# Kernel optimization log

Hardware: AMD Instinct MI355X
Metric: run time of the kernel (lower is better)

## Reference

```python
import jax, jax.numpy as jnp
import numpy as np

B, C, H, W = 512, 64, 32, 64
NUM_NODE = 128


def setup_inputs() -> dict:
    key = jax.random.key(0)
    ks = jax.random.split(key, 11)
    f = jnp.float32
    def nrm(k, shape, s):
        return jax.random.normal(k, shape, f) * s
    return {
        "x":   jax.random.normal(ks[0], (B, C, H, W), f),
        "w11": nrm(ks[1], (32, 64, 1, 1), 0.1), "b11": nrm(ks[2], (32,), 0.05),
        "w12": nrm(ks[3], (16, 32, 3, 3), 0.1), "b12": nrm(ks[4], (16,), 0.05),
        "w21": nrm(ks[5], (8, 16, 1, 1), 0.1),  "b21": nrm(ks[6], (8,), 0.05),
        "w22": nrm(ks[7], (4, 8, 3, 3), 0.1),   "b22": nrm(ks[8], (4,), 0.05),
        "fcw": nrm(ks[9], (2 * NUM_NODE, 32 * 64 * 4), 0.05),
        "fcb": nrm(ks[10], (2 * NUM_NODE,), 0.05),
    }


def _conv_relu(x, w, b, pad):
    y = jax.lax.conv_general_dilated(
        x, w, window_strides=(1, 1), padding=[(pad, pad), (pad, pad)],
        dimension_numbers=("NCHW", "OIHW", "NCHW"))
    return jax.nn.relu(y + b[None, :, None, None])


def reference(x, w11, b11, w12, b12, w21, b21, w22, b22, fcw, fcb):
    # --- GraphGen3: conv stack -> fc -> n_Sigmoid -> [B, N, 2] ---
    h = _conv_relu(x, w11, b11, 0)
    h = _conv_relu(h, w12, b12, 1)
    h = _conv_relu(h, w21, b21, 0)
    h = _conv_relu(h, w22, b22, 1)          # [B, 4, 32, 64]
    z = h.reshape(h.shape[0], -1) @ fcw.T + fcb  # [B, 2N]
    c01 = jax.nn.sigmoid(3.0 * z).reshape(x.shape[0], -1, 2)  # n_Sigmoid(x, 3)
    # --- get_coord: scale normalized coords to pixel range ---
    Hd, Wd = x.shape[2], x.shape[3]
    coord = c01 * jnp.array([Hd - 1, Wd - 1], x.dtype)  # [B, N, 2]
    # --- th_batch_map_coordinates: clamp, corner gather, bilinear lerp ---
    ch = jnp.clip(coord[..., 0], 0.0, Hd - 1)
    cw = jnp.clip(coord[..., 1], 0.0, Wd - 1)
    h0 = jnp.floor(ch).astype(jnp.int32); h1 = jnp.ceil(ch).astype(jnp.int32)
    w0 = jnp.floor(cw).astype(jnp.int32); w1 = jnp.ceil(cw).astype(jnp.int32)
    bidx = jnp.arange(x.shape[0])[:, None]  # [B, 1]
    def gv(hi, wi):
        return x[bidx, :, hi, wi]           # gather -> [B, N, C]
    v_lt = gv(h0, w0); v_rt = gv(h1, w0)
    v_lb = gv(h0, w1); v_rb = gv(h1, w1)
    oh = (ch - h0.astype(x.dtype))[..., None]
    ow = (cw - w0.astype(x.dtype))[..., None]
    vt = v_lt + oh * (v_rt - v_lt)
    vb = v_lb + oh * (v_rb - v_lb)
    graph_feat = vt + ow * (vb - vt)        # [B, N, C] (matches permute(0,2,1))
    return graph_feat, coord
```

## Files before the change

kernel.cpp:

```cpp
#include <hip/hip_runtime.h>
#include <cstdint>

#define BATCH 512
#define CIN   64
#define HH    32
#define WW    64
#define HW    2048
#define C1    32
#define C2    16
#define C3    8
#define C4    4
#define NOUT  256
#define KFC   8192
#define NODES 128
#define KS    32
#define GF_SIZE (BATCH * NODES * CIN)

typedef __attribute__((ext_vector_type(8))) short bfrag;
typedef __attribute__((ext_vector_type(4))) float ffrag;

__device__ __forceinline__ ushort bf_trunc(float f) { return (ushort)(__float_as_uint(f) >> 16); }
__device__ __forceinline__ float  bf_truncf(float f) { return __uint_as_float(__float_as_uint(f) & 0xffff0000u); }
__device__ __forceinline__ ushort f2bf(float f) {
  uint32_t u = __float_as_uint(f);
  return (ushort)((u + 0x7fffu + ((u >> 16) & 1u)) >> 16);
}
__device__ __forceinline__ uint32_t pack2(float a, float b) {
  return (uint32_t)f2bf(a) | ((uint32_t)f2bf(b) << 16);
}
__device__ __forceinline__ uint32_t packhi2(float a, float b) {
  return (uint32_t)bf_trunc(a) | ((uint32_t)bf_trunc(b) << 16);
}

__global__ __launch_bounds__(256) void k_conv12(
    const float* __restrict__ x, const float* __restrict__ w11, const float* __restrict__ b11,
    const float* __restrict__ w12, const float* __restrict__ b12,
    float* __restrict__ h2, int b0)
{
  __shared__ __align__(16) char h1s[10 * 66 * 64];
  const int tid = threadIdx.x;
  const int l   = tid & 63;
  const int wv  = tid >> 6;
  const int lr  = l & 15;
  const int lg  = l >> 4;
  const int r0  = blockIdx.x * 8;
  const int bg  = b0 + blockIdx.y;
  const float* xb = x + (size_t)bg * CIN * HW;

  if (tid < 160) {
    int row = tid >> 4, half = (tid >> 3) & 1, q = tid & 7;
    int cell = row * 66 + (half ? 65 : 0);
    *(uint2*)(h1s + (cell << 6) + q * 8) = uint2{0u, 0u};
  }

  bfrag w1h[2][2], w1l[2][2];
  #pragma unroll
  for (int m = 0; m < 2; ++m) {
    #pragma unroll
    for (int ks = 0; ks < 2; ++ks) {
      const float* wp = w11 + (m * 16 + lr) * 64 + ks * 32 + lg * 8;
      #pragma unroll
      for (int e = 0; e < 8; ++e) {
        float v = wp[e];
        w1h[m][ks][e] = (short)bf_trunc(v);
        w1l[m][ks][e] = (short)f2bf(v - bf_truncf(v));
      }
    }
  }
  float bias1[2][4];
  #pragma unroll
  for (int m = 0; m < 2; ++m) {
    #pragma unroll
    for (int r = 0; r < 4; ++r) bias1[m][r] = b11[m * 16 + lg * 4 + r];
  }

  #pragma unroll 2
  for (int i = 0; i < 10; ++i) {
    const int nt   = wv * 10 + i;
    const int ry   = nt >> 2;
    const int col0 = (nt & 3) << 4;
    const int y    = r0 - 1 + ry;
    const int colb = col0 + 1 + lr;
    if (y >= 0 && y < HH) {
      float xv[16];
      const float* xp = xb + y * WW + col0 + lr;
      #pragma unroll
      for (int ks = 0; ks < 2; ++ks) {
        #pragma unroll
        for (int e = 0; e < 8; ++e)
          xv[ks * 8 + e] = xp[(ks * 32 + lg * 8 + e) * HW];
      }
      bfrag xh[2], xl[2];
      #pragma unroll
      for (int ks = 0; ks < 2; ++ks) {
        #pragma unroll
        for (int e = 0; e < 8; ++e) {
          float v = xv[ks * 8 + e];
          xh[ks][e] = (short)bf_trunc(v);
          xl[ks][e] = (short)f2bf(v - bf_truncf(v));
        }
      }
      ffrag a0 = {0.f, 0.f, 0.f, 0.f}, a1 = {0.f, 0.f, 0.f, 0.f};
      #pragma unroll
      for (int ks = 0; ks < 2; ++ks) {
        a0 = __builtin_amdgcn_mfma_f32_16x16x32_bf16(w1h[0][ks], xh[ks], a0, 0, 0, 0);
        a0 = __builtin_amdgcn_mfma_f32_16x16x32_bf16(w1h[0][ks], xl[ks], a0, 0, 0, 0);
        a0 = __builtin_amdgcn_mfma_f32_16x16x32_bf16(w1l[0][ks], xh[ks], a0, 0, 0, 0);
        a1 = __builtin_amdgcn_mfma_f32_16x16x32_bf16(w1h[1][ks], xh[ks], a1, 0, 0, 0);
        a1 = __builtin_amdgcn_mfma_f32_16x16x32_bf16(w1h[1][ks], xl[ks], a1, 0, 0, 0);
        a1 = __builtin_amdgcn_mfma_f32_16x16x32_bf16(w1l[1][ks], xh[ks], a1, 0, 0, 0);
      }
      #pragma unroll
      for (int m = 0; m < 2; ++m) {
        float v0 = fmaxf((m ? a1[0] : a0[0]) + bias1[m][0], 0.f);
        float v1 = fmaxf((m ? a1[1] : a0[1]) + bias1[m][1], 0.f);
        float v2 = fmaxf((m ? a1[2] : a0[2]) + bias1[m][2], 0.f);
        float v3 = fmaxf((m ? a1[3] : a0[3]) + bias1[m][3], 0.f);
        int chunk = (m * 2 + (lg >> 1)) ^ ((colb >> 1) & 3);
        char* dst = h1s + ((ry * 66 + colb) << 6) + (chunk << 4) + (lg & 1) * 8;
        *(uint2*)dst = uint2{pack2(v0, v1), pack2(v2, v3)};
      }
    } else {
      #pragma unroll
      for (int m = 0; m < 2; ++m) {
        int chunk = (m * 2 + (lg >> 1)) ^ ((colb >> 1) & 3);
        char* dst = h1s + ((ry * 66 + colb) << 6) + (chunk << 4) + (lg & 1) * 8;
        *(uint2*)dst = uint2{0u, 0u};
      }
    }
  }
  __syncthreads();

  bfrag w2h[9], w2l[9];
  #pragma unroll
  for (int t = 0; t < 9; ++t) {
    const float* wp = w12 + lr * 288 + t;
    #pragma unroll
    for (int e = 0; e < 8; ++e) {
      float v = wp[(lg * 8 + e) * 9];
      w2h[t][e] = (short)bf_trunc(v);
      w2l[t][e] = (short)f2bf(v - bf_truncf(v));
    }
  }
  float bias2[4];
  #pragma unroll
  for (int r = 0; r < 4; ++r) bias2[r] = b12[lg * 4 + r];

  #pragma unroll 2
  for (int i = 0; i < 8; ++i) {
    const int nt   = wv * 8 + i;
    const int ryo  = nt >> 2;
    const int col0 = (nt & 3) << 4;
    ffrag acc = {0.f, 0.f, 0.f, 0.f};
    #pragma unroll
    for (int ky = 0; ky < 3; ++ky) {
      const int row = ryo + ky;
      #pragma unroll
      for (int kx = 0; kx < 3; ++kx) {
        const int colb  = col0 + lr + kx;
        const int chunk = lg ^ ((colb >> 1) & 3);
        const bfrag hv = *(const bfrag*)(h1s + ((row * 66 + colb) << 6) + (chunk << 4));
        acc = __builtin_amdgcn_mfma_f32_16x16x32_bf16(w2h[ky * 3 + kx], hv, acc, 0, 0, 0);
        acc = __builtin_amdgcn_mfma_f32_16x16x32_bf16(w2l[ky * 3 + kx], hv, acc, 0, 0, 0);
      }
    }
    const int px = (r0 + ryo) * WW + col0 + lr;
    float4 o;
    o.x = fmaxf(acc[0] + bias2[0], 0.f);
    o.y = fmaxf(acc[1] + bias2[1], 0.f);
    o.z = fmaxf(acc[2] + bias2[2], 0.f);
    o.w = fmaxf(acc[3] + bias2[3], 0.f);
    *(float4*)(h2 + ((size_t)blockIdx.y * HW + px) * 16 + lg * 4) = o;
  }
}

__global__ __launch_bounds__(256) void k_conv34(
    const float* __restrict__ h2, const float* __restrict__ w21, const float* __restrict__ b21,
    const float* __restrict__ w22, const float* __restrict__ b22,
    ushort* __restrict__ h4h, ushort* __restrict__ h4l)
{
  __shared__ float h3s[18][64][9];
  __shared__ float __align__(16) w21s[128];
  __shared__ float __align__(16) w22s[288];
  const int tid = threadIdx.x;
  const int r0  = blockIdx.x * 16;
  const size_t b = blockIdx.y;

  for (int i = tid; i < 128; i += 256) w21s[(i & 15) * 8 + (i >> 4)] = w21[i];
  for (int i = tid; i < 288; i += 256) {
    int o = i / 72, r = i - o * 72, c = r / 9, tap = r - c * 9;
    w22s[(tap * 8 + c) * 4 + o] = w22[i];
  }
  __syncthreads();

  for (int p = tid; p < 18 * 64; p += 256) {
    const int ry = p >> 6, wc = p & 63;
    const int y  = r0 - 1 + ry;
    float* hd = &h3s[ry][wc][0];
    if (y >= 0 && y < HH) {
      const float4* hp = (const float4*)(h2 + ((b * HH + y) * WW + wc) * C2);
      float4 v0 = hp[0], v1 = hp[1], v2 = hp[2], v3 = hp[3];
      float xv[16] = {v0.x, v0.y, v0.z, v0.w, v1.x, v1.y, v1.z, v1.w,
                      v2.x, v2.y, v2.z, v2.w, v3.x, v3.y, v3.z, v3.w};
      float acc[C3];
      #pragma unroll
      for (int o = 0; o < C3; ++o) acc[o] = b21[o];
      #pragma unroll
      for (int c = 0; c < 16; ++c) {
        const float4* wr = (const float4*)&w21s[c * 8];
        float4 a = wr[0], d = wr[1];
        float v = xv[c];
        acc[0] = fmaf(v, a.x, acc[0]); acc[1] = fmaf(v, a.y, acc[1]);
        acc[2] = fmaf(v, a.z, acc[2]); acc[3] = fmaf(v, a.w, acc[3]);
        acc[4] = fmaf(v, d.x, acc[4]); acc[5] = fmaf(v, d.y, acc[5]);
        acc[6] = fmaf(v, d.z, acc[6]); acc[7] = fmaf(v, d.w, acc[7]);
      }
      #pragma unroll
      for (int c = 0; c < C3; ++c) hd[c] = fmaxf(acc[c], 0.f);
    } else {
      #pragma unroll
      for (int c = 0; c < C3; ++c) hd[c] = 0.f;
    }
  }
  __syncthreads();

  for (int p = tid; p < 1024; p += 256) {
    const int yl = p >> 6, wc = p & 63, ry = yl + 1;
    float acc[C4] = {b22[0], b22[1], b22[2], b22[3]};
    #pragma unroll
    for (int ky = 0; ky < 3; ++ky) {
      #pragma unroll
      for (int kx = 0; kx < 3; ++kx) {
        const int wcc = wc + kx - 1;
        if (wcc < 0 || wcc >= WW) continue;
        const float* hb = &h3s[ry + ky - 1][wcc][0];
        const int tap = ky * 3 + kx;
        #pragma unroll
        for (int c = 0; c < C3; ++c) {
          float v = hb[c];
          float4 w4 = *(const float4*)&w22s[(tap * 8 + c) * 4];
          acc[0] = fmaf(v, w4.x, acc[0]); acc[1] = fmaf(v, w4.y, acc[1]);
          acc[2] = fmaf(v, w4.z, acc[2]); acc[3] = fmaf(v, w4.w, acc[3]);
        }
      }
    }
    const size_t base = b * KFC + (r0 + yl) * WW + wc;
    #pragma unroll
    for (int o = 0; o < C4; ++o) {
      float v = fmaxf(acc[o], 0.f);
      h4h[base + (size_t)o * HW] = bf_trunc(v);
      h4l[base + (size_t)o * HW] = f2bf(v - bf_truncf(v));
    }
  }
}

__global__ __launch_bounds__(256) void k_cvt_fcw(
    const float* __restrict__ w, ushort* __restrict__ hi, ushort* __restrict__ lo)
{
  const int i = (blockIdx.x * 256 + threadIdx.x) * 8;
  const float4 a = *(const float4*)(w + i);
  const float4 b = *(const float4*)(w + i + 4);
  uint4 hv, lv;
  hv.x = packhi2(a.x, a.y); hv.y = packhi2(a.z, a.w);
  hv.z = packhi2(b.x, b.y); hv.w = packhi2(b.z, b.w);
  lv.x = pack2(a.x - bf_truncf(a.x), a.y - bf_truncf(a.y));
  lv.y = pack2(a.z - bf_truncf(a.z), a.w - bf_truncf(a.w));
  lv.z = pack2(b.x - bf_truncf(b.x), b.y - bf_truncf(b.y));
  lv.w = pack2(b.z - bf_truncf(b.z), b.w - bf_truncf(b.w));
  *(uint4*)(hi + i) = hv;
  *(uint4*)(lo + i) = lv;
}

__global__ __launch_bounds__(256) void k_fc(
    const ushort* __restrict__ Ahp, const ushort* __restrict__ Alp,
    const ushort* __restrict__ Bhp, const ushort* __restrict__ Blp,
    float* __restrict__ zpart, int cb)
{
  const int tid = threadIdx.x;
  const int l   = tid & 63;
  const int wv  = tid >> 6;
  const int lr  = l & 15;
  const int lg  = l >> 4;
  const int m0  = blockIdx.x * 64 + (wv >> 1) * 32;
  const int n0  = blockIdx.y * 64 + (wv & 1) * 32;
  const int k0  = blockIdx.z * (KFC / KS);

  int mrow[2], nrow[2];
  #pragma unroll
  for (int t = 0; t < 2; ++t) {
    int m = m0 + t * 16 + lr;
    mrow[t] = m < cb ? m : cb - 1;
    nrow[t] = n0 + t * 16 + lr;
  }
  ffrag acc[2][2] = {};

  #pragma unroll 1
  for (int kc = 0; kc < (KFC / KS) / 32; ++kc) {
    const int k = k0 + kc * 32 + lg * 8;
    bfrag ah[2], al[2], bh[2], bl[2];
    #pragma unroll
    for (int t = 0; t < 2; ++t) {
      ah[t] = *(const bfrag*)(Ahp + (size_t)mrow[t] * KFC + k);
      al[t] = *(const bfrag*)(Alp + (size_t)mrow[t] * KFC + k);
      bh[t] = *(const bfrag*)(Bhp + (size_t)nrow[t] * KFC + k);
      bl[t] = *(const bfrag*)(Blp + (size_t)nrow[t] * KFC + k);
    }
    #pragma unroll
    for (int mt = 0; mt < 2; ++mt) {
      #pragma unroll
      for (int nt = 0; nt < 2; ++nt) {
        acc[mt][nt] = __builtin_amdgcn_mfma_f32_16x16x32_bf16(ah[mt], bh[nt], acc[mt][nt], 0, 0, 0);
        acc[mt][nt] = __builtin_amdgcn_mfma_f32_16x16x32_bf16(ah[mt], bl[nt], acc[mt][nt], 0, 0, 0);
        acc[mt][nt] = __builtin_amdgcn_mfma_f32_16x16x32_bf16(al[mt], bh[nt], acc[mt][nt], 0, 0, 0);
      }
    }
  }

  #pragma unroll
  for (int mt = 0; mt < 2; ++mt) {
    #pragma unroll
    for (int r = 0; r < 4; ++r) {
      const int m = m0 + mt * 16 + lg * 4 + r;
      if (m < cb) {
        #pragma unroll
        for (int nt = 0; nt < 2; ++nt)
          zpart[((size_t)blockIdx.z * cb + m) * NOUT + n0 + nt * 16 + lr] = acc[mt][nt][r];
      }
    }
  }
}

__global__ __launch_bounds__(256) void k_coord(
    const float* __restrict__ zpart, const float* __restrict__ fcb,
    float* __restrict__ out, int cb, int b0)
{
  const int b = blockIdx.x;
  const int o = threadIdx.x;
  float z = fcb[o];
  #pragma unroll 8
  for (int kb = 0; kb < KS; ++kb) z += zpart[((size_t)kb * cb + b) * NOUT + o];
  float s = 1.f / (1.f + __expf(-3.f * z));
  const int node = o >> 1, comp = o & 1;
  out[GF_SIZE + (((size_t)(b0 + b) * NODES + node) << 1) + comp] = s * (comp ? 63.f : 31.f);
}

__global__ __launch_bounds__(256) void k_gather(
    const float* __restrict__ x, float* __restrict__ out, int b0, int cb)
{
  const int bid = blockIdx.x;
  int bl, g;
  if ((cb & 7) == 0) {
    const int xcd = bid & 7;
    const int j   = bid >> 3;
    g  = j & 31;
    bl = (j >> 5) * 8 + xcd;
  } else {
    bl = bid >> 5;
    g  = bid & 31;
  }
  const int node = g * 4 + (threadIdx.x >> 6);
  const int c    = threadIdx.x & 63;
  const int bg   = b0 + bl;
  const float* cp = out + GF_SIZE + ((size_t)bg * NODES + node) * 2;
  float chv = fminf(fmaxf(cp[0], 0.f), 31.f);
  float cwv = fminf(fmaxf(cp[1], 0.f), 63.f);
  float fh = floorf(chv), fw = floorf(cwv);
  int h0 = (int)fh, h1i = (int)ceilf(chv);
  int w0 = (int)fw, w1i = (int)ceilf(cwv);
  float oh = chv - fh, ow = cwv - fw;
  const float* xb = x + ((size_t)bg * CIN + c) * HW;
  float v_lt = xb[h0 * WW + w0];
  float v_rt = xb[h1i * WW + w0];
  float v_lb = xb[h0 * WW + w1i];
  float v_rb = xb[h1i * WW + w1i];
  float vt = v_lt + oh * (v_rt - v_lt);
  float vb = v_lb + oh * (v_rb - v_lb);
  out[((size_t)bg * NODES + node) * CIN + c] = vt + ow * (vb - vt);
}

extern "C" void kernel_launch(void* const* d_in, const int* in_sizes, int n_in,
                              void* d_out, int out_size, void* d_ws, size_t ws_size,
                              hipStream_t stream)
{
  (void)in_sizes; (void)n_in; (void)out_size;
  const float* x   = (const float*)d_in[0];
  const float* w11 = (const float*)d_in[1];
  const float* b11 = (const float*)d_in[2];
  const float* w12 = (const float*)d_in[3];
  const float* b12 = (const float*)d_in[4];
  const float* w21 = (const float*)d_in[5];
  const float* b21 = (const float*)d_in[6];
  const float* w22 = (const float*)d_in[7];
  const float* b22 = (const float*)d_in[8];
  const float* fcw = (const float*)d_in[9];
  const float* fcb = (const float*)d_in[10];
  float* out = (float*)d_out;
  char* wsb  = (char*)d_ws;

  const size_t perB  = 131072 + 16384 + 16384 + (size_t)KS * NOUT * 4;
  const size_t fixed = 2 * 4194304;
  size_t avail = ws_size > fixed ? ws_size - fixed : perB;
  size_t cbmax = avail / perB;
  int CB = (int)(cbmax < (size_t)BATCH ? cbmax : (size_t)BATCH);
  if (CB < 1) CB = 1;

  char* p = wsb;
  float*  h2v  = (float*)p;   p += (size_t)CB * 131072;
  ushort* h4h  = (ushort*)p;  p += (size_t)CB * 16384;
  ushort* h4l  = (ushort*)p;  p += (size_t)CB * 16384;
  float*  zpv  = (float*)p;   p += (size_t)CB * KS * NOUT * 4;
  ushort* fcwh = (ushort*)p;  p += 4194304;
  ushort* fcwl = (ushort*)p;

  k_cvt_fcw<<<dim3(NOUT * KFC / (256 * 8)), 256, 0, stream>>>(fcw, fcwh, fcwl);

  for (int b0 = 0; b0 < BATCH; b0 += CB) {
    const int cb = (BATCH - b0 < CB) ? (BATCH - b0) : CB;
    k_conv12<<<dim3(4, cb), 256, 0, stream>>>(x, w11, b11, w12, b12, h2v, b0);
    k_conv34<<<dim3(2, cb), 256, 0, stream>>>(h2v, w21, b21, w22, b22, h4h, h4l);
    k_fc<<<dim3((cb + 63) / 64, 4, KS), 256, 0, stream>>>(h4h, h4l, fcwh, fcwl, zpv, cb);
    k_coord<<<dim3(cb), 256, 0, stream>>>(zpv, fcb, out, cb, b0);
    k_gather<<<dim3(cb * 32), 256, 0, stream>>>(x, out, b0, cb);
  }
}
```

Baseline: 254.0 us.

## Fuse coord into gather, halve FC split-K, drop x low-part MFMA in conv1

```diff
diff --git a/kernel.cpp b/kernel.cpp
--- a/kernel.cpp
+++ b/kernel.cpp
@@ -13,7 +13,7 @@
 #define NOUT  256
 #define KFC   8192
 #define NODES 128
-#define KS    32
+#define KS    16
 #define GF_SIZE (BATCH * NODES * CIN)
 
 typedef __attribute__((ext_vector_type(8))) short bfrag;
@@ -82,32 +82,20 @@
     const int y    = r0 - 1 + ry;
     const int colb = col0 + 1 + lr;
     if (y >= 0 && y < HH) {
-      float xv[16];
       const float* xp = xb + y * WW + col0 + lr;
+      bfrag xh[2];
       #pragma unroll
       for (int ks = 0; ks < 2; ++ks) {
         #pragma unroll
         for (int e = 0; e < 8; ++e)
-          xv[ks * 8 + e] = xp[(ks * 32 + lg * 8 + e) * HW];
-      }
-      bfrag xh[2], xl[2];
-      #pragma unroll
-      for (int ks = 0; ks < 2; ++ks) {
-        #pragma unroll
-        for (int e = 0; e < 8; ++e) {
-          float v = xv[ks * 8 + e];
-          xh[ks][e] = (short)bf_trunc(v);
-          xl[ks][e] = (short)f2bf(v - bf_truncf(v));
-        }
+          xh[ks][e] = (short)f2bf(xp[(ks * 32 + lg * 8 + e) * HW]);
       }
       ffrag a0 = {0.f, 0.f, 0.f, 0.f}, a1 = {0.f, 0.f, 0.f, 0.f};
       #pragma unroll
       for (int ks = 0; ks < 2; ++ks) {
         a0 = __builtin_amdgcn_mfma_f32_16x16x32_bf16(w1h[0][ks], xh[ks], a0, 0, 0, 0);
-        a0 = __builtin_amdgcn_mfma_f32_16x16x32_bf16(w1h[0][ks], xl[ks], a0, 0, 0, 0);
         a0 = __builtin_amdgcn_mfma_f32_16x16x32_bf16(w1l[0][ks], xh[ks], a0, 0, 0, 0);
         a1 = __builtin_amdgcn_mfma_f32_16x16x32_bf16(w1h[1][ks], xh[ks], a1, 0, 0, 0);
-        a1 = __builtin_amdgcn_mfma_f32_16x16x32_bf16(w1h[1][ks], xl[ks], a1, 0, 0, 0);
         a1 = __builtin_amdgcn_mfma_f32_16x16x32_bf16(w1l[1][ks], xh[ks], a1, 0, 0, 0);
       }
       #pragma unroll
@@ -330,22 +318,9 @@
   }
 }
 
-__global__ __launch_bounds__(256) void k_coord(
-    const float* __restrict__ zpart, const float* __restrict__ fcb,
-    float* __restrict__ out, int cb, int b0)
-{
-  const int b = blockIdx.x;
-  const int o = threadIdx.x;
-  float z = fcb[o];
-  #pragma unroll 8
-  for (int kb = 0; kb < KS; ++kb) z += zpart[((size_t)kb * cb + b) * NOUT + o];
-  float s = 1.f / (1.f + __expf(-3.f * z));
-  const int node = o >> 1, comp = o & 1;
-  out[GF_SIZE + (((size_t)(b0 + b) * NODES + node) << 1) + comp] = s * (comp ? 63.f : 31.f);
-}
-
 __global__ __launch_bounds__(256) void k_gather(
-    const float* __restrict__ x, float* __restrict__ out, int b0, int cb)
+    const float* __restrict__ x, const float* __restrict__ zpart,
+    const float* __restrict__ fcb, float* __restrict__ out, int cb, int b0)
 {
   const int bid = blockIdx.x;
   int bl, g;
@@ -359,23 +334,38 @@
     g  = bid & 31;
   }
   const int node = g * 4 + (threadIdx.x >> 6);
-  const int c    = threadIdx.x & 63;
+  const int l    = threadIdx.x & 63;
   const int bg   = b0 + bl;
-  const float* cp = out + GF_SIZE + ((size_t)bg * NODES + node) * 2;
-  float chv = fminf(fmaxf(cp[0], 0.f), 31.f);
-  float cwv = fminf(fmaxf(cp[1], 0.f), 63.f);
-  float fh = floorf(chv), fw = floorf(cwv);
-  int h0 = (int)fh, h1i = (int)ceilf(chv);
-  int w0 = (int)fw, w1i = (int)ceilf(cwv);
-  float oh = chv - fh, ow = cwv - fw;
-  const float* xb = x + ((size_t)bg * CIN + c) * HW;
-  float v_lt = xb[h0 * WW + w0];
-  float v_rt = xb[h1i * WW + w0];
-  float v_lb = xb[h0 * WW + w1i];
-  float v_rb = xb[h1i * WW + w1i];
-  float vt = v_lt + oh * (v_rt - v_lt);
-  float vb = v_lb + oh * (v_rb - v_lb);
-  out[((size_t)bg * NODES + node) * CIN + c] = vt + ow * (vb - vt);
+
+  float val = 0.f;
+  if (l < 2 * KS) {
+    const int kb = l >> 1, comp = l & 1;
+    val = zpart[((size_t)kb * cb + bl) * NOUT + node * 2 + comp];
+  }
+  #pragma unroll
+  for (int off = 2; off < 2 * KS; off <<= 1) val += __shfl_xor(val, off);
+  const float z0 = __shfl(val, 0) + fcb[node * 2 + 0];
+  const float z1 = __shfl(val, 1) + fcb[node * 2 + 1];
+  const float ch = 31.f / (1.f + __expf(-3.f * z0));
+  const float cw = 63.f / (1.f + __expf(-3.f * z1));
+
+  if (l < 2)
+    out[GF_SIZE + (((size_t)bg * NODES + node) << 1) + l] = l ? cw : ch;
+
+  const float chv = fminf(fmaxf(ch, 0.f), 31.f);
+  const float cwv = fminf(fmaxf(cw, 0.f), 63.f);
+  const float fh = floorf(chv), fw = floorf(cwv);
+  const int h0 = (int)fh, h1i = (int)ceilf(chv);
+  const int w0 = (int)fw, w1i = (int)ceilf(cwv);
+  const float oh = chv - fh, ow = cwv - fw;
+  const float* xb = x + ((size_t)bg * CIN + l) * HW;
+  const float v_lt = xb[h0 * WW + w0];
+  const float v_rt = xb[h1i * WW + w0];
+  const float v_lb = xb[h0 * WW + w1i];
+  const float v_rb = xb[h1i * WW + w1i];
+  const float vt = v_lt + oh * (v_rt - v_lt);
+  const float vb = v_lb + oh * (v_rb - v_lb);
+  out[((size_t)bg * NODES + node) * CIN + l] = vt + ow * (vb - vt);
 }
 
 extern "C" void kernel_launch(void* const* d_in, const int* in_sizes, int n_in,
@@ -419,7 +409,6 @@
     k_conv12<<<dim3(4, cb), 256, 0, stream>>>(x, w11, b11, w12, b12, h2v, b0);
     k_conv34<<<dim3(2, cb), 256, 0, stream>>>(h2v, w21, b21, w22, b22, h4h, h4l);
     k_fc<<<dim3((cb + 63) / 64, 4, KS), 256, 0, stream>>>(h4h, h4l, fcwh, fcwl, zpv, cb);
-    k_coord<<<dim3(cb), 256, 0, stream>>>(zpv, fcb, out, cb, b0);
-    k_gather<<<dim3(cb * 32), 256, 0, stream>>>(x, out, b0, cb);
-  }
-}
+    k_gather<<<dim3(cb * 32), 256, 0, stream>>>(x, zpv, fcb, out, cb, b0);
+  }
+}
```

Result: slower. 263.1 us (+3.6%).
